# Performance work log

Measured on AMD Instinct MI355X. Metric: run time of the kernel, lower is better.

The kernel has to match this reference:

```python
import jax, jax.numpy as jnp
import numpy as np

H = 4096      # hidden_size
F = 14336     # intermediate_size (ffn)
GS = 64       # HQQ group_size along axis 0 (output rows)
NB = 4        # nbits
T = 512       # tokens routed to this expert


def _make_qlinear(key, N, K):
    """Quantized weight of logical shape (N, K) = (out, in), HQQ axis=0 groups."""
    k1, k2, k3 = jax.random.split(key, 3)
    W_q = jax.random.randint(k1, (N, K), 0, 2 ** NB, dtype=jnp.int32)
    scale = jax.random.uniform(k2, (N // GS, K), dtype=jnp.float32) * 0.02 + 1e-3
    zero = jax.random.uniform(k3, (N // GS, K), dtype=jnp.float32) * (2.0 ** (NB - 1))
    return W_q, scale, zero


def setup_inputs() -> dict:
    key = jax.random.key(0)
    kx, k1, k2, k3 = jax.random.split(key, 4)
    w1_q, w1_scale, w1_zero = _make_qlinear(k1, F, H)  # gate proj
    w2_q, w2_scale, w2_zero = _make_qlinear(k2, H, F)  # down proj
    w3_q, w3_scale, w3_zero = _make_qlinear(k3, F, H)  # up proj
    hidden_states = jax.random.normal(kx, (T, H), dtype=jnp.float32)
    return dict(hidden_states=hidden_states,
                w1_q=w1_q, w1_scale=w1_scale, w1_zero=w1_zero,
                w2_q=w2_q, w2_scale=w2_scale, w2_zero=w2_zero,
                w3_q=w3_q, w3_scale=w3_scale, w3_zero=w3_zero)


def _dequant(W_q, scale, zero):
    # W[n, k] = (W_q[n, k] - zero[n // GS, k]) * scale[n // GS, k]
    N, K = W_q.shape
    Wf = W_q.reshape(N // GS, GS, K).astype(scale.dtype)
    return ((Wf - zero[:, None, :]) * scale[:, None, :]).reshape(N, K)


def reference(hidden_states,
              w1_q, w1_scale, w1_zero,
              w2_q, w2_scale, w2_zero,
              w3_q, w3_scale, w3_zero):
    gate = hidden_states @ _dequant(w1_q, w1_scale, w1_zero).T  # [T, F]
    up = hidden_states @ _dequant(w3_q, w3_scale, w3_zero).T    # [T, F]
    inter = jax.nn.silu(gate) * up                               # [T, F]
    return inter @ _dequant(w2_q, w2_scale, w2_zero).T           # [T, H]
```

## Files before the change

### kernel.cpp

```cpp
#include <hip/hip_runtime.h>
#include <stdint.h>

typedef __bf16 bf16;
typedef __attribute__((ext_vector_type(8))) bf16 bf16x8;
typedef __attribute__((ext_vector_type(4))) bf16 bf16x4;
typedef __attribute__((ext_vector_type(4))) float f32x4;

#define T_DIM 512
#define H_DIM 4096
#define F_DIM 14336

__device__ __forceinline__ int swz(int r, int c) {
    return r * 64 + (c ^ ((r & 7) << 3));
}

__device__ __forceinline__ int xcd_remap(int d, int chunk) {
    return (d & 7) * chunk + (d >> 3);
}

__device__ __forceinline__ void barrier_nodrain() {
    __builtin_amdgcn_sched_barrier(0);
    asm volatile("s_waitcnt lgkmcnt(0)\n\ts_barrier" ::: "memory");
    __builtin_amdgcn_sched_barrier(0);
}

__global__ void cvt_x_kernel(const float* __restrict__ x, bf16* __restrict__ xb) {
    int i = (blockIdx.x * 256 + threadIdx.x) * 4;
    float4 v = *(const float4*)(x + i);
    bf16x4 o = {(bf16)v.x, (bf16)v.y, (bf16)v.z, (bf16)v.w};
    *(bf16x4*)(xb + i) = o;
}

__global__ __launch_bounds__(256, 2)
void gemm_gateup(const bf16* __restrict__ A,
                 const int* __restrict__ Wq1, const float* __restrict__ Sc1,
                 const float* __restrict__ Zr1,
                 const int* __restrict__ Wq3, const float* __restrict__ Sc3,
                 const float* __restrict__ Zr3,
                 bf16* __restrict__ inter) {
    constexpr int KD = H_DIM;
    constexpr int NT = KD / 64;
    __shared__ __align__(16) bf16 As[2][128 * 64];
    __shared__ __align__(16) bf16 Bs1[2][64 * 64];
    __shared__ __align__(16) bf16 Bs3[2][64 * 64];

    const int l    = xcd_remap(blockIdx.x, 112);
    const int bx   = l & 3;
    const int by   = l >> 2;
    const int tid  = threadIdx.x;
    const int lane = tid & 63;
    const int wid  = tid >> 6;
    const int wm   = wid >> 1, wn = wid & 1;
    const int lr   = lane & 15;
    const int lk   = (lane >> 4) * 8;
    const int m0   = bx * 128;
    const int n0   = by * 64;
    const int grp  = by;

    const int a_r = tid >> 2;
    const int a_c = (tid & 3) * 8;
    const int b_r = (tid >> 4) * 4;
    const int b_c = (tid & 15) * 4;

    f32x4 acc1[4][2], acc3[4][2];
    const f32x4 zf = {0.f, 0.f, 0.f, 0.f};
#pragma unroll
    for (int i = 0; i < 4; i++)
#pragma unroll
        for (int j = 0; j < 2; j++) { acc1[i][j] = zf; acc3[i][j] = zf; }

    bf16x8 areg[4];
    int4   q1r[4], q3r[4];
    float4 s1r, z1r, s3r, z3r;

#define STAGE(K0)                                                                 \
    {                                                                             \
        _Pragma("unroll")                                                         \
        for (int p = 0; p < 2; p++)                                               \
            _Pragma("unroll")                                                     \
            for (int h = 0; h < 2; h++)                                           \
                areg[p * 2 + h] = *(const bf16x8*)(A + (size_t)(m0 + a_r + 64 * p) * KD + (K0) + a_c + 32 * h); \
        _Pragma("unroll")                                                         \
        for (int i = 0; i < 4; i++) {                                             \
            q1r[i] = *(const int4*)(Wq1 + (size_t)(n0 + b_r + i) * KD + (K0) + b_c); \
            q3r[i] = *(const int4*)(Wq3 + (size_t)(n0 + b_r + i) * KD + (K0) + b_c); \
        }                                                                         \
        s1r = *(const float4*)(Sc1 + (size_t)grp * KD + (K0) + b_c);              \
        z1r = *(const float4*)(Zr1 + (size_t)grp * KD + (K0) + b_c);              \
        s3r = *(const float4*)(Sc3 + (size_t)grp * KD + (K0) + b_c);              \
        z3r = *(const float4*)(Zr3 + (size_t)grp * KD + (K0) + b_c);              \
    }

#define WLDS(nb)                                                                  \
    {                                                                             \
        _Pragma("unroll")                                                         \
        for (int p = 0; p < 2; p++)                                               \
            _Pragma("unroll")                                                     \
            for (int h = 0; h < 2; h++)                                           \
                *(bf16x8*)&As[nb][swz(a_r + 64 * p, a_c + 32 * h)] = areg[p * 2 + h]; \
        float4 n1, n3;                                                            \
        n1.x = -z1r.x * s1r.x; n1.y = -z1r.y * s1r.y;                             \
        n1.z = -z1r.z * s1r.z; n1.w = -z1r.w * s1r.w;                             \
        n3.x = -z3r.x * s3r.x; n3.y = -z3r.y * s3r.y;                             \
        n3.z = -z3r.z * s3r.z; n3.w = -z3r.w * s3r.w;                             \
        _Pragma("unroll")                                                         \
        for (int i = 0; i < 4; i++) {                                             \
            bf16x4 v;                                                             \
            v[0] = (bf16)fmaf((float)q1r[i].x, s1r.x, n1.x);                      \
            v[1] = (bf16)fmaf((float)q1r[i].y, s1r.y, n1.y);                      \
            v[2] = (bf16)fmaf((float)q1r[i].z, s1r.z, n1.z);                      \
            v[3] = (bf16)fmaf((float)q1r[i].w, s1r.w, n1.w);                      \
            *(bf16x4*)&Bs1[nb][swz(b_r + i, b_c)] = v;                            \
            bf16x4 u;                                                             \
            u[0] = (bf16)fmaf((float)q3r[i].x, s3r.x, n3.x);                      \
            u[1] = (bf16)fmaf((float)q3r[i].y, s3r.y, n3.y);                      \
            u[2] = (bf16)fmaf((float)q3r[i].z, s3r.z, n3.z);                      \
            u[3] = (bf16)fmaf((float)q3r[i].w, s3r.w, n3.w);                      \
            *(bf16x4*)&Bs3[nb][swz(b_r + i, b_c)] = u;                            \
        }                                                                         \
    }

    STAGE(0);
    WLDS(0);
    STAGE(64);
    barrier_nodrain();

    for (int t = 0; t < NT; ++t) {
        const int cur = t & 1;
#pragma unroll
        for (int kk = 0; kk < 2; kk++) {
            bf16x8 af[4], b1[2], b3[2];
#pragma unroll
            for (int mi = 0; mi < 4; mi++)
                af[mi] = *(const bf16x8*)&As[cur][swz(wm * 64 + mi * 16 + lr, kk * 32 + lk)];
#pragma unroll
            for (int ni = 0; ni < 2; ni++) {
                b1[ni] = *(const bf16x8*)&Bs1[cur][swz(wn * 32 + ni * 16 + lr, kk * 32 + lk)];
                b3[ni] = *(const bf16x8*)&Bs3[cur][swz(wn * 32 + ni * 16 + lr, kk * 32 + lk)];
            }
#pragma unroll
            for (int mi = 0; mi < 4; mi++)
#pragma unroll
                for (int ni = 0; ni < 2; ni++) {
                    acc1[mi][ni] = __builtin_amdgcn_mfma_f32_16x16x32_bf16(af[mi], b1[ni], acc1[mi][ni], 0, 0, 0);
                    acc3[mi][ni] = __builtin_amdgcn_mfma_f32_16x16x32_bf16(af[mi], b3[ni], acc3[mi][ni], 0, 0, 0);
                }
        }
        if (t + 1 < NT) {
            WLDS(cur ^ 1);
            if (t + 2 < NT) STAGE((t + 2) * 64);
            barrier_nodrain();
        }
    }
#undef STAGE
#undef WLDS

    const int orow = (lane >> 4) * 4;
#pragma unroll
    for (int mi = 0; mi < 4; mi++)
#pragma unroll
        for (int ni = 0; ni < 2; ni++) {
#pragma unroll
            for (int r = 0; r < 4; r++) {
                int m = m0 + wm * 64 + mi * 16 + orow + r;
                int c = n0 + wn * 32 + ni * 16 + lr;
                float g = acc1[mi][ni][r];
                float u = acc3[mi][ni][r];
                float s = g / (1.0f + __expf(-g));
                inter[(size_t)m * F_DIM + c] = (bf16)(s * u);
            }
        }
}

template<int SPLITK>
__global__ __launch_bounds__(256, 3)
void gemm_down(const bf16* __restrict__ A, const int* __restrict__ Wq,
               const float* __restrict__ Sc, const float* __restrict__ Zr,
               float* __restrict__ partials) {
    constexpr int KD = F_DIM;
    constexpr int KC = KD / SPLITK;
    constexpr int NT = KC / 64;
    __shared__ __align__(16) bf16 As[2][128 * 64];
    __shared__ __align__(16) bf16 Bs[2][64 * 64];

    const int l    = xcd_remap(blockIdx.x, 32 * SPLITK);
    const int bx   = l & 3;
    const int by   = (l >> 2) & 63;
    const int bz   = l >> 8;
    const int tid  = threadIdx.x;
    const int lane = tid & 63;
    const int wid  = tid >> 6;
    const int wm   = wid >> 1, wn = wid & 1;
    const int lr   = lane & 15;
    const int lk   = (lane >> 4) * 8;
    const int m0   = bx * 128;
    const int n0   = by * 64;
    const int grp  = by;
    const int kbeg = bz * KC;

    const int a_r = tid >> 2;
    const int a_c = (tid & 3) * 8;
    const int b_r = (tid >> 4) * 4;
    const int b_c = (tid & 15) * 4;

    f32x4 acc[4][2];
    const f32x4 zf = {0.f, 0.f, 0.f, 0.f};
#pragma unroll
    for (int i = 0; i < 4; i++)
#pragma unroll
        for (int j = 0; j < 2; j++) acc[i][j] = zf;

    bf16x8 areg[4];
    int4   qr[4];
    float4 sr, zr;

#define STAGE(K0)                                                                 \
    {                                                                             \
        _Pragma("unroll")                                                         \
        for (int p = 0; p < 2; p++)                                               \
            _Pragma("unroll")                                                     \
            for (int h = 0; h < 2; h++)                                           \
                areg[p * 2 + h] = *(const bf16x8*)(A + (size_t)(m0 + a_r + 64 * p) * KD + kbeg + (K0) + a_c + 32 * h); \
        _Pragma("unroll")                                                         \
        for (int i = 0; i < 4; i++)                                               \
            qr[i] = *(const int4*)(Wq + (size_t)(n0 + b_r + i) * KD + kbeg + (K0) + b_c); \
        sr = *(const float4*)(Sc + (size_t)grp * KD + kbeg + (K0) + b_c);         \
        zr = *(const float4*)(Zr + (size_t)grp * KD + kbeg + (K0) + b_c);         \
    }

#define WLDS(nb)                                                                  \
    {                                                                             \
        _Pragma("unroll")                                                         \
        for (int p = 0; p < 2; p++)                                               \
            _Pragma("unroll")                                                     \
            for (int h = 0; h < 2; h++)                                           \
                *(bf16x8*)&As[nb][swz(a_r + 64 * p, a_c + 32 * h)] = areg[p * 2 + h]; \
        float4 nz;                                                                \
        nz.x = -zr.x * sr.x; nz.y = -zr.y * sr.y;                                 \
        nz.z = -zr.z * sr.z; nz.w = -zr.w * sr.w;                                 \
        _Pragma("unroll")                                                         \
        for (int i = 0; i < 4; i++) {                                             \
            bf16x4 v;                                                             \
            v[0] = (bf16)fmaf((float)qr[i].x, sr.x, nz.x);                        \
            v[1] = (bf16)fmaf((float)qr[i].y, sr.y, nz.y);                        \
            v[2] = (bf16)fmaf((float)qr[i].z, sr.z, nz.z);                        \
            v[3] = (bf16)fmaf((float)qr[i].w, sr.w, nz.w);                        \
            *(bf16x4*)&Bs[nb][swz(b_r + i, b_c)] = v;                             \
        }                                                                         \
    }

    STAGE(0);
    WLDS(0);
    STAGE(64);
    barrier_nodrain();

    for (int t = 0; t < NT; ++t) {
        const int cur = t & 1;
#pragma unroll
        for (int kk = 0; kk < 2; kk++) {
            bf16x8 af[4], bfr[2];
#pragma unroll
            for (int mi = 0; mi < 4; mi++)
                af[mi] = *(const bf16x8*)&As[cur][swz(wm * 64 + mi * 16 + lr, kk * 32 + lk)];
#pragma unroll
            for (int ni = 0; ni < 2; ni++)
                bfr[ni] = *(const bf16x8*)&Bs[cur][swz(wn * 32 + ni * 16 + lr, kk * 32 + lk)];
#pragma unroll
            for (int mi = 0; mi < 4; mi++)
#pragma unroll
                for (int ni = 0; ni < 2; ni++)
                    acc[mi][ni] = __builtin_amdgcn_mfma_f32_16x16x32_bf16(af[mi], bfr[ni], acc[mi][ni], 0, 0, 0);
        }
        if (t + 1 < NT) {
            WLDS(cur ^ 1);
            if (t + 2 < NT) STAGE((t + 2) * 64);
            barrier_nodrain();
        }
    }
#undef STAGE
#undef WLDS

    float* po = partials + (size_t)bz * T_DIM * H_DIM;
    const int orow = (lane >> 4) * 4;
#pragma unroll
    for (int mi = 0; mi < 4; mi++)
#pragma unroll
        for (int ni = 0; ni < 2; ni++) {
#pragma unroll
            for (int r = 0; r < 4; r++) {
                int m = m0 + wm * 64 + mi * 16 + orow + r;
                int c = n0 + wn * 32 + ni * 16 + lr;
                po[(size_t)m * H_DIM + c] = acc[mi][ni][r];
            }
        }
}

template<int S>
__global__ void reduce_kernel(const float* __restrict__ partials, float* __restrict__ out) {
    size_t i = ((size_t)blockIdx.x * 256 + threadIdx.x) * 4;
    f32x4 a = *(const f32x4*)(partials + i);
#pragma unroll
    for (int s = 1; s < S; s++)
        a += *(const f32x4*)(partials + (size_t)s * T_DIM * H_DIM + i);
    *(f32x4*)(out + i) = a;
}

extern "C" void kernel_launch(void* const* d_in, const int* in_sizes, int n_in,
                              void* d_out, int out_size, void* d_ws, size_t ws_size,
                              hipStream_t stream) {
    const float* x   = (const float*)d_in[0];
    const int*   w1q = (const int*)d_in[1];
    const float* w1s = (const float*)d_in[2];
    const float* w1z = (const float*)d_in[3];
    const int*   w2q = (const int*)d_in[4];
    const float* w2s = (const float*)d_in[5];
    const float* w2z = (const float*)d_in[6];
    const int*   w3q = (const int*)d_in[7];
    const float* w3s = (const float*)d_in[8];
    const float* w3z = (const float*)d_in[9];

    bf16*  xb    = (bf16*)d_ws;
    bf16*  inter = xb + (size_t)T_DIM * H_DIM;
    float* parts = (float*)(inter + (size_t)T_DIM * F_DIM);

    const size_t base   = (size_t)T_DIM * H_DIM * 2 + (size_t)T_DIM * F_DIM * 2;
    const size_t pbytes = (size_t)T_DIM * H_DIM * 4;

    cvt_x_kernel<<<dim3(2048), dim3(256), 0, stream>>>(x, xb);

    gemm_gateup<<<dim3(896), dim3(256), 0, stream>>>(
        xb, w1q, w1s, w1z, w3q, w3s, w3z, inter);

    if (ws_size >= base + 4 * pbytes) {
        gemm_down<4><<<dim3(1024), dim3(256), 0, stream>>>(inter, w2q, w2s, w2z, parts);
        reduce_kernel<4><<<dim3(2048), dim3(256), 0, stream>>>(parts, (float*)d_out);
    } else if (ws_size >= base + 2 * pbytes) {
        gemm_down<2><<<dim3(512), dim3(256), 0, stream>>>(inter, w2q, w2s, w2z, parts);
        reduce_kernel<2><<<dim3(2048), dim3(256), 0, stream>>>(parts, (float*)d_out);
    } else {
        gemm_down<1><<<dim3(256), dim3(256), 0, stream>>>(inter, w2q, w2s, w2z, parts);
        reduce_kernel<1><<<dim3(2048), dim3(256), 0, stream>>>(parts, (float*)d_out);
    }
}
```

Baseline: 381.4 us.

## Deepen weight prefetch to two stages with ping-pong register buffers

Splits the staging step so quantized weight tiles are fetched into two alternating register buffers, two K-tiles ahead, while activations and scales stay one tile ahead. The main loop is unrolled by two so each phase uses a fixed LDS buffer and register set. The aim is to hide more global-load latency on the weight stream in both the gate/up and down-proj kernels. In exchange it adds VGPR pressure, which may lower occupancy, and the unrolled loop assumes an even number of K tiles.

```diff
diff --git a/kernel.cpp b/kernel.cpp
--- a/kernel.cpp
+++ b/kernel.cpp
@@ -70,28 +70,33 @@
         for (int j = 0; j < 2; j++) { acc1[i][j] = zf; acc3[i][j] = zf; }
 
     bf16x8 areg[4];
-    int4   q1r[4], q3r[4];
+    int4   qa1[4], qa3[4];
+    int4   qb1[4], qb3[4];
     float4 s1r, z1r, s3r, z3r;
 
-#define STAGE(K0)                                                                 \
+#define ASZ(K0)                                                                   \
     {                                                                             \
         _Pragma("unroll")                                                         \
         for (int p = 0; p < 2; p++)                                               \
             _Pragma("unroll")                                                     \
             for (int h = 0; h < 2; h++)                                           \
                 areg[p * 2 + h] = *(const bf16x8*)(A + (size_t)(m0 + a_r + 64 * p) * KD + (K0) + a_c + 32 * h); \
-        _Pragma("unroll")                                                         \
-        for (int i = 0; i < 4; i++) {                                             \
-            q1r[i] = *(const int4*)(Wq1 + (size_t)(n0 + b_r + i) * KD + (K0) + b_c); \
-            q3r[i] = *(const int4*)(Wq3 + (size_t)(n0 + b_r + i) * KD + (K0) + b_c); \
-        }                                                                         \
         s1r = *(const float4*)(Sc1 + (size_t)grp * KD + (K0) + b_c);              \
         z1r = *(const float4*)(Zr1 + (size_t)grp * KD + (K0) + b_c);              \
         s3r = *(const float4*)(Sc3 + (size_t)grp * KD + (K0) + b_c);              \
         z3r = *(const float4*)(Zr3 + (size_t)grp * KD + (K0) + b_c);              \
     }
 
-#define WLDS(nb)                                                                  \
+#define QST(Q1, Q3, K0)                                                           \
+    {                                                                             \
+        _Pragma("unroll")                                                         \
+        for (int i = 0; i < 4; i++) {                                             \
+            Q1[i] = *(const int4*)(Wq1 + (size_t)(n0 + b_r + i) * KD + (K0) + b_c); \
+            Q3[i] = *(const int4*)(Wq3 + (size_t)(n0 + b_r + i) * KD + (K0) + b_c); \
+        }                                                                         \
+    }
+
+#define WLDS(Q1, Q3, nb)                                                          \
     {                                                                             \
         _Pragma("unroll")                                                         \
         for (int p = 0; p < 2; p++)                                               \
@@ -106,54 +111,71 @@
         _Pragma("unroll")                                                         \
         for (int i = 0; i < 4; i++) {                                             \
             bf16x4 v;                                                             \
-            v[0] = (bf16)fmaf((float)q1r[i].x, s1r.x, n1.x);                      \
-            v[1] = (bf16)fmaf((float)q1r[i].y, s1r.y, n1.y);                      \
-            v[2] = (bf16)fmaf((float)q1r[i].z, s1r.z, n1.z);                      \
-            v[3] = (bf16)fmaf((float)q1r[i].w, s1r.w, n1.w);                      \
+            v[0] = (bf16)fmaf((float)Q1[i].x, s1r.x, n1.x);                       \
+            v[1] = (bf16)fmaf((float)Q1[i].y, s1r.y, n1.y);                       \
+            v[2] = (bf16)fmaf((float)Q1[i].z, s1r.z, n1.z);                       \
+            v[3] = (bf16)fmaf((float)Q1[i].w, s1r.w, n1.w);                       \
             *(bf16x4*)&Bs1[nb][swz(b_r + i, b_c)] = v;                            \
             bf16x4 u;                                                             \
-            u[0] = (bf16)fmaf((float)q3r[i].x, s3r.x, n3.x);                      \
-            u[1] = (bf16)fmaf((float)q3r[i].y, s3r.y, n3.y);                      \
-            u[2] = (bf16)fmaf((float)q3r[i].z, s3r.z, n3.z);                      \
-            u[3] = (bf16)fmaf((float)q3r[i].w, s3r.w, n3.w);                      \
+            u[0] = (bf16)fmaf((float)Q3[i].x, s3r.x, n3.x);                       \
+            u[1] = (bf16)fmaf((float)Q3[i].y, s3r.y, n3.y);                       \
+            u[2] = (bf16)fmaf((float)Q3[i].z, s3r.z, n3.z);                       \
+            u[3] = (bf16)fmaf((float)Q3[i].w, s3r.w, n3.w);                       \
             *(bf16x4*)&Bs3[nb][swz(b_r + i, b_c)] = u;                            \
         }                                                                         \
     }
 
-    STAGE(0);
-    WLDS(0);
-    STAGE(64);
+#define MFMA_PH(nb)                                                               \
+    {                                                                             \
+        _Pragma("unroll")                                                         \
+        for (int kk = 0; kk < 2; kk++) {                                          \
+            bf16x8 af[4], b1[2], b3[2];                                           \
+            _Pragma("unroll")                                                     \
+            for (int mi = 0; mi < 4; mi++)                                        \
+                af[mi] = *(const bf16x8*)&As[nb][swz(wm * 64 + mi * 16 + lr, kk * 32 + lk)]; \
+            _Pragma("unroll")                                                     \
+            for (int ni = 0; ni < 2; ni++) {                                      \
+                b1[ni] = *(const bf16x8*)&Bs1[nb][swz(wn * 32 + ni * 16 + lr, kk * 32 + lk)]; \
+                b3[ni] = *(const bf16x8*)&Bs3[nb][swz(wn * 32 + ni * 16 + lr, kk * 32 + lk)]; \
+            }                                                                     \
+            _Pragma("unroll")                                                     \
+            for (int mi = 0; mi < 4; mi++)                                        \
+                _Pragma("unroll")                                                 \
+                for (int ni = 0; ni < 2; ni++) {                                  \
+                    acc1[mi][ni] = __builtin_amdgcn_mfma_f32_16x16x32_bf16(af[mi], b1[ni], acc1[mi][ni], 0, 0, 0); \
+                    acc3[mi][ni] = __builtin_amdgcn_mfma_f32_16x16x32_bf16(af[mi], b3[ni], acc3[mi][ni], 0, 0, 0); \
+                }                                                                 \
+        }                                                                         \
+    }
+
+    ASZ(0);
+    QST(qa1, qa3, 0);
+    WLDS(qa1, qa3, 0);
+    ASZ(64);
+    QST(qb1, qb3, 64);
+    QST(qa1, qa3, 128);
     barrier_nodrain();
 
-    for (int t = 0; t < NT; ++t) {
-        const int cur = t & 1;
-#pragma unroll
-        for (int kk = 0; kk < 2; kk++) {
-            bf16x8 af[4], b1[2], b3[2];
-#pragma unroll
-            for (int mi = 0; mi < 4; mi++)
-                af[mi] = *(const bf16x8*)&As[cur][swz(wm * 64 + mi * 16 + lr, kk * 32 + lk)];
-#pragma unroll
-            for (int ni = 0; ni < 2; ni++) {
-                b1[ni] = *(const bf16x8*)&Bs1[cur][swz(wn * 32 + ni * 16 + lr, kk * 32 + lk)];
-                b3[ni] = *(const bf16x8*)&Bs3[cur][swz(wn * 32 + ni * 16 + lr, kk * 32 + lk)];
-            }
-#pragma unroll
-            for (int mi = 0; mi < 4; mi++)
-#pragma unroll
-                for (int ni = 0; ni < 2; ni++) {
-                    acc1[mi][ni] = __builtin_amdgcn_mfma_f32_16x16x32_bf16(af[mi], b1[ni], acc1[mi][ni], 0, 0, 0);
-                    acc3[mi][ni] = __builtin_amdgcn_mfma_f32_16x16x32_bf16(af[mi], b3[ni], acc3[mi][ni], 0, 0, 0);
-                }
-        }
-        if (t + 1 < NT) {
-            WLDS(cur ^ 1);
-            if (t + 2 < NT) STAGE((t + 2) * 64);
+    for (int t = 0; t < NT; t += 2) {
+        MFMA_PH(0);
+        {
+            WLDS(qb1, qb3, 1);
+            if (t + 2 < NT) ASZ((t + 2) * 64);
+            if (t + 3 < NT) QST(qb1, qb3, (t + 3) * 64);
             barrier_nodrain();
         }
-    }
-#undef STAGE
+        MFMA_PH(1);
+        if (t + 2 < NT) {
+            WLDS(qa1, qa3, 0);
+            if (t + 3 < NT) ASZ((t + 3) * 64);
+            if (t + 4 < NT) QST(qa1, qa3, (t + 4) * 64);
+            barrier_nodrain();
+        }
+    }
+#undef ASZ
+#undef QST
 #undef WLDS
+#undef MFMA_PH
 
     const int orow = (lane >> 4) * 4;
 #pragma unroll
@@ -211,24 +233,28 @@
         for (int j = 0; j < 2; j++) acc[i][j] = zf;
 
     bf16x8 areg[4];
-    int4   qr[4];
+    int4   qa[4], qb[4];
     float4 sr, zr;
 
-#define STAGE(K0)                                                                 \
+#define ASZ(K0)                                                                   \
     {                                                                             \
         _Pragma("unroll")                                                         \
         for (int p = 0; p < 2; p++)                                               \
             _Pragma("unroll")                                                     \
             for (int h = 0; h < 2; h++)                                           \
                 areg[p * 2 + h] = *(const bf16x8*)(A + (size_t)(m0 + a_r + 64 * p) * KD + kbeg + (K0) + a_c + 32 * h); \
-        _Pragma("unroll")                                                         \
-        for (int i = 0; i < 4; i++)                                               \
-            qr[i] = *(const int4*)(Wq + (size_t)(n0 + b_r + i) * KD + kbeg + (K0) + b_c); \
         sr = *(const float4*)(Sc + (size_t)grp * KD + kbeg + (K0) + b_c);         \
         zr = *(const float4*)(Zr + (size_t)grp * KD + kbeg + (K0) + b_c);         \
     }
 
-#define WLDS(nb)                                                                  \
+#define QST(Q, K0)                                                                \
+    {                                                                             \
+        _Pragma("unroll")                                                         \
+        for (int i = 0; i < 4; i++)                                               \
+            Q[i] = *(const int4*)(Wq + (size_t)(n0 + b_r + i) * KD + kbeg + (K0) + b_c); \
+    }
+
+#define WLDS(Q, nb)                                                               \
     {                                                                             \
         _Pragma("unroll")                                                         \
         for (int p = 0; p < 2; p++)                                               \
@@ -241,44 +267,61 @@
         _Pragma("unroll")                                                         \
         for (int i = 0; i < 4; i++) {                                             \
             bf16x4 v;                                                             \
-            v[0] = (bf16)fmaf((float)qr[i].x, sr.x, nz.x);                        \
-            v[1] = (bf16)fmaf((float)qr[i].y, sr.y, nz.y);                        \
-            v[2] = (bf16)fmaf((float)qr[i].z, sr.z, nz.z);                        \
-            v[3] = (bf16)fmaf((float)qr[i].w, sr.w, nz.w);                        \
+            v[0] = (bf16)fmaf((float)Q[i].x, sr.x, nz.x);                         \
+            v[1] = (bf16)fmaf((float)Q[i].y, sr.y, nz.y);                         \
+            v[2] = (bf16)fmaf((float)Q[i].z, sr.z, nz.z);                         \
+            v[3] = (bf16)fmaf((float)Q[i].w, sr.w, nz.w);                         \
             *(bf16x4*)&Bs[nb][swz(b_r + i, b_c)] = v;                             \
         }                                                                         \
     }
 
-    STAGE(0);
-    WLDS(0);
-    STAGE(64);
+#define MFMA_PH(nb)                                                               \
+    {                                                                             \
+        _Pragma("unroll")                                                         \
+        for (int kk = 0; kk < 2; kk++) {                                          \
+            bf16x8 af[4], bfr[2];                                                 \
+            _Pragma("unroll")                                                     \
+            for (int mi = 0; mi < 4; mi++)                                        \
+                af[mi] = *(const bf16x8*)&As[nb][swz(wm * 64 + mi * 16 + lr, kk * 32 + lk)]; \
+            _Pragma("unroll")                                                     \
+            for (int ni = 0; ni < 2; ni++)                                        \
+                bfr[ni] = *(const bf16x8*)&Bs[nb][swz(wn * 32 + ni * 16 + lr, kk * 32 + lk)]; \
+            _Pragma("unroll")                                                     \
+            for (int mi = 0; mi < 4; mi++)                                        \
+                _Pragma("unroll")                                                 \
+                for (int ni = 0; ni < 2; ni++)                                    \
+                    acc[mi][ni] = __builtin_amdgcn_mfma_f32_16x16x32_bf16(af[mi], bfr[ni], acc[mi][ni], 0, 0, 0); \
+        }                                                                         \
+    }
+
+    ASZ(0);
+    QST(qa, 0);
+    WLDS(qa, 0);
+    ASZ(64);
+    QST(qb, 64);
+    QST(qa, 128);
     barrier_nodrain();
 
-    for (int t = 0; t < NT; ++t) {
-        const int cur = t & 1;
-#pragma unroll
-        for (int kk = 0; kk < 2; kk++) {
-            bf16x8 af[4], bfr[2];
-#pragma unroll
-            for (int mi = 0; mi < 4; mi++)
-                af[mi] = *(const bf16x8*)&As[cur][swz(wm * 64 + mi * 16 + lr, kk * 32 + lk)];
-#pragma unroll
-            for (int ni = 0; ni < 2; ni++)
-                bfr[ni] = *(const bf16x8*)&Bs[cur][swz(wn * 32 + ni * 16 + lr, kk * 32 + lk)];
-#pragma unroll
-            for (int mi = 0; mi < 4; mi++)
-#pragma unroll
-                for (int ni = 0; ni < 2; ni++)
-                    acc[mi][ni] = __builtin_amdgcn_mfma_f32_16x16x32_bf16(af[mi], bfr[ni], acc[mi][ni], 0, 0, 0);
-        }
-        if (t + 1 < NT) {
-            WLDS(cur ^ 1);
-            if (t + 2 < NT) STAGE((t + 2) * 64);
+    for (int t = 0; t < NT; t += 2) {
+        MFMA_PH(0);
+        {
+            WLDS(qb, 1);
+            if (t + 2 < NT) ASZ((t + 2) * 64);
+            if (t + 3 < NT) QST(qb, (t + 3) * 64);
             barrier_nodrain();
         }
-    }
-#undef STAGE
+        MFMA_PH(1);
+        if (t + 2 < NT) {
+            WLDS(qa, 0);
+            if (t + 3 < NT) ASZ((t + 3) * 64);
+            if (t + 4 < NT) QST(qa, (t + 4) * 64);
+            barrier_nodrain();
+        }
+    }
+#undef ASZ
+#undef QST
 #undef WLDS
+#undef MFMA_PH
 
     float* po = partials + (size_t)bz * T_DIM * H_DIM;
     const int orow = (lane >> 4) * 4;
```

After: 381.3 us. Within noise of the previous version (-0.0%).
